# Optimization experiments

Hardware: AMD Instinct MI355X
Metric: run time of the kernel (lower is better)

## Reference

```python
import jax, jax.numpy as jnp
import numpy as np

ADMP = 8  # admp_channel -> K = ADMP*ADMP keypoints


def setup_inputs() -> dict:
    key = jax.random.key(0)
    kA, kB = jax.random.split(key)
    B, C, H, W = 8, 512, 96, 96
    feature_A = jax.random.normal(kA, (B, C, H, W), dtype=jnp.float32)
    feature_B = jax.random.normal(kB, (B, C, H, W), dtype=jnp.float32)
    return {"feature_A": feature_A, "feature_B": feature_B}


def _keypoint_rowcol(feature_A):
    # featureSelect: sum over channels, AdaptiveMaxPool2d(ADMP) with return_indices.
    # H,W divisible by ADMP so adaptive pool == uniform non-overlapping pooling.
    B, C, H, W = feature_A.shape
    ph, pw = H // ADMP, W // ADMP
    resp = feature_A.sum(axis=1)  # [B,H,W]
    r = resp.reshape(B, ADMP, ph, ADMP, pw).transpose(0, 1, 3, 2, 4)
    r = r.reshape(B, ADMP * ADMP, ph * pw)
    loc = jnp.argmax(r, axis=-1)  # first-max, matches torch  [B,K]
    kk = jnp.arange(ADMP * ADMP)
    gi, gj = kk // ADMP, kk % ADMP
    row_A = gi[None, :] * ph + loc // pw  # [B,K]
    col_A = gj[None, :] * pw + loc % pw
    return row_A, col_A


def reference(feature_A, feature_B):
    B, C, H, W = feature_A.shape
    K = ADMP * ADMP
    row_A, col_A = _keypoint_rowcol(feature_A)
    flat_A = row_A * W + col_A  # [B,K]

    # gather descriptors: [B,K,C]
    fa = feature_A.reshape(B, C, H * W)
    desc = jnp.take_along_axis(fa, flat_A[:, None, :], axis=2).transpose(0, 2, 1)

    # squared L2 distance map via ||b||^2 - 2 a.b + ||a||^2 : [B,K,HW]
    fb = feature_B.reshape(B, C, H * W)
    fb_sq = jnp.sum(fb * fb, axis=1)            # [B,HW]
    d_sq = jnp.sum(desc * desc, axis=-1)        # [B,K]
    cross = jnp.einsum('bkc,bcn->bkn', desc, fb)  # [B,K,HW]
    dist = fb_sq[:, None, :] - 2.0 * cross + d_sq[:, :, None]

    min_idx = jnp.argmin(dist, axis=-1)  # [B,K]
    row_B = min_idx // W
    col_B = min_idx % W
    drow = -(row_B - row_A)
    dcol = -(col_B - col_A)
    off = jnp.stack([drow, dcol], axis=-1)  # [B,K,2] int

    # getTranslationalOffsetByMode: most frequent (drow,dcol) pair per batch
    eq = jnp.all(off[:, :, None, :] == off[:, None, :, :], axis=-1)  # [B,K,K]
    counts = eq.sum(axis=-1)  # [B,K]
    best = jnp.argmax(counts, axis=-1)  # first occurrence on ties, matches dict order
    out = jnp.take_along_axis(off, best[:, None, None], axis=1)[:, 0, :]  # [B,2]
    return out
```

## Files before the change

kernel.cpp:

```cpp
#include <hip/hip_runtime.h>
#include <hip/hip_bf16.h>
#include <math.h>

typedef _Float16 half8 __attribute__((ext_vector_type(8)));
typedef __fp16 fp16x2 __attribute__((ext_vector_type(2)));
typedef float f32x4 __attribute__((ext_vector_type(4)));
typedef unsigned short u16x4 __attribute__((ext_vector_type(4)));
typedef unsigned short u16x8 __attribute__((ext_vector_type(8)));
typedef unsigned long long u64;

#define B_   8
#define C_   512
#define H_   96
#define W_   96
#define HW   9216
#define K_   64
#define PH   12
#define PW   12
#define NT   96
#define CCH  32
#define NBLK 96

#define OFF_PARTIAL 0u
#define OFF_DESCH   2359296u
#define OFF_DESCL   2883584u
#define OFF_ROWA    3407872u
#define OFF_COLA    3409920u
#define OFF_SLOTS   3411968u

#define FBT_LO 3072
#define BUFHW  6144

__global__ __launch_bounds__(256) void k_partial(const float* __restrict__ A,
                                                 float* __restrict__ part,
                                                 u64* __restrict__ slots) {
    if (blockIdx.x == 0 && blockIdx.y == 0) {
        slots[threadIdx.x] = ~0ull;
        slots[threadIdx.x + 256] = ~0ull;
    }
    int bxs = (blockIdx.x & 7) * 9 + (blockIdx.x >> 3);
    int idx4 = bxs * 256 + threadIdx.x;
    int chunk = blockIdx.y;
    int b = idx4 / (HW / 4), hw4 = idx4 - b * (HW / 4);
    const float* p = A + ((size_t)(b * C_ + chunk * 64)) * HW + hw4 * 4;
    float4 s = make_float4(0.f, 0.f, 0.f, 0.f);
#pragma unroll
    for (int i = 0; i < 64; ++i) {
        float4 v = *(const float4*)&p[(size_t)i * HW];
        s.x += v.x; s.y += v.y; s.z += v.z; s.w += v.w;
    }
    *(float4*)&part[chunk * (B_ * HW) + b * HW + hw4 * 4] = s;
}

__global__ void k_selgather(const float* __restrict__ part, const float* __restrict__ A,
                            int* __restrict__ rowA, int* __restrict__ colA,
                            _Float16* __restrict__ descH, _Float16* __restrict__ descL) {
    int k = blockIdx.x, b = blockIdx.y, lane = threadIdx.x;
    int gi = k >> 3, gj = k & 7;
    float bv = -1e30f; int bp = 1 << 20;
    for (int p = lane; p < PH * PW; p += 64) {
        int lr = p / PW, lc = p - lr * PW;
        int hw = (gi * PH + lr) * W_ + gj * PW + lc;
        float v = 0.f;
#pragma unroll
        for (int ch = 0; ch < 8; ++ch) v += part[ch * (B_ * HW) + b * HW + hw];
        if (v > bv || (v == bv && p < bp)) { bv = v; bp = p; }
    }
    for (int m = 1; m < 64; m <<= 1) {
        float ov = __shfl_xor(bv, m);
        int   op = __shfl_xor(bp, m);
        if (ov > bv || (ov == bv && op < bp)) { bv = ov; bp = op; }
    }
    int lr = bp / PW, lc = bp - lr * PW;
    int r = gi * PH + lr, c = gj * PW + lc;
    int flat = r * W_ + c;
    if (lane == 0) { rowA[b * K_ + k] = r; colA[b * K_ + k] = c; }
#pragma unroll
    for (int i = 0; i < 8; ++i) {
        int cc = i * 64 + lane;
        float v = A[((size_t)(b * C_ + cc)) * HW + flat];
        _Float16 h = (_Float16)v;
        _Float16 lo = (_Float16)((v - (float)h) * 2048.f);
        size_t o = ((size_t)(b * K_ + k)) * C_ + cc;
        descH[o] = h; descL[o] = lo;
    }
}

__global__ __launch_bounds__(256, 3) void k_main(const float* __restrict__ FB,
                                                 const _Float16* __restrict__ descH,
                                                 const _Float16* __restrict__ descL,
                                                 u64* __restrict__ slots) {
    __shared__ __attribute__((aligned(16))) unsigned short smem_us[2 * BUFHW];
    int b = blockIdx.y;
    int bxs = (blockIdx.x & 7) * 12 + (blockIdx.x >> 3);
    int nb = bxs * NT;
    int tid = threadIdx.x;
    int l = tid & 63;
    int w = tid >> 6;
    const size_t baseB = (size_t)b * C_ * HW + nb;

    const int so = tid % 12;
    const int scb = tid / 12;
    const int st_nt = so >> 1, st_nn0 = (so & 1) * 8;
    const size_t dbase = ((size_t)(b * K_) + w * 16 + (l & 15)) * C_ + (l >> 4) * 8;

    f32x4 accH[6], accX[6];
#pragma unroll
    for (int nt = 0; nt < 6; ++nt) {
        accH[nt] = (f32x4){0.f, 0.f, 0.f, 0.f};
        accX[nt] = (f32x4){0.f, 0.f, 0.f, 0.f};
    }
    float sq[8];
#pragma unroll
    for (int j = 0; j < 8; ++j) sq[j] = 0.f;

    float4 r0a, r0b, r1a, r1b;
    u16x8 AdH, AdL, BdH, BdL;

#define LOADFB(c0)                                                            \
    do {                                                                      \
        if (tid < 192) {                                                      \
            const float* p0 = &FB[baseB + (size_t)((c0) + scb) * HW + so * 8];      \
            const float* p1 = &FB[baseB + (size_t)((c0) + scb + 16) * HW + so * 8]; \
            r0a = *(const float4*)p0; r0b = *(const float4*)(p0 + 4);         \
            r1a = *(const float4*)p1; r1b = *(const float4*)(p1 + 4);         \
        }                                                                     \
    } while (0)

#define LOADDESC(S, c0)                                                       \
    do {                                                                      \
        S##dH = *(const u16x8*)&descH[dbase + (c0)];                          \
        S##dL = *(const u16x8*)&descL[dbase + (c0)];                          \
    } while (0)

#define CVT8(va, vb, hofs)                                                    \
    do {                                                                      \
        union { fp16x2 p[4]; half8 h; } hh, ll;                               \
        float vv[8] = {va.x, va.y, va.z, va.w, vb.x, vb.y, vb.z, vb.w};       \
        _Pragma("unroll")                                                     \
        for (int j = 0; j < 4; ++j) {                                         \
            float a = vv[2 * j], bq = vv[2 * j + 1];                          \
            fp16x2 hp = __builtin_amdgcn_cvt_pkrtz(a, bq);                    \
            float ha = (float)hp[0], hb = (float)hp[1];                       \
            fp16x2 lp = __builtin_amdgcn_cvt_pkrtz((a - ha) * 2048.f,         \
                                                   (bq - hb) * 2048.f);       \
            hh.p[j] = hp; ll.p[j] = lp;                                       \
            sq[2 * j]     = fmaf(a, a, sq[2 * j]);                            \
            sq[2 * j + 1] = fmaf(bq, bq, sq[2 * j + 1]);                      \
        }                                                                     \
        *(half8*)&smem_us[(hofs)] = hh.h;                                     \
        *(half8*)&smem_us[(hofs) + FBT_LO] = ll.h;                            \
    } while (0)

#define WRITEFB(bufhw)                                                        \
    do {                                                                      \
        if (tid < 192) {                                                      \
            int c = scb;                                                      \
            int off0 = (bufhw) + st_nt * 512 + ((c >> 2) & 1) * 256           \
                       + (c >> 3) * 64 + (c & 3) * 16 + st_nn0;               \
            CVT8(r0a, r0b, off0);                                             \
            c = scb + 16;                                                     \
            int off1 = (bufhw) + st_nt * 512 + ((c >> 2) & 1) * 256           \
                       + (c >> 3) * 64 + (c & 3) * 16 + st_nn0;               \
            CVT8(r1a, r1b, off1);                                             \
        }                                                                     \
    } while (0)

    const unsigned lds0 = (unsigned)(size_t)&smem_us[0];

#define TRQ(d0, d1, d2, d3, addr)                                             \
    asm volatile("ds_read_b64_tr_b16 %0, %1"             : "=v"(d0) : "v"(addr)); \
    asm volatile("ds_read_b64_tr_b16 %0, %1 offset:512"  : "=v"(d1) : "v"(addr)); \
    asm volatile("ds_read_b64_tr_b16 %0, %1 offset:6144" : "=v"(d2) : "v"(addr)); \
    asm volatile("ds_read_b64_tr_b16 %0, %1 offset:6656" : "=v"(d3) : "v"(addr));

#define WAIT8 asm volatile("s_waitcnt lgkmcnt(8)" ::: "memory");              \
              __builtin_amdgcn_sched_barrier(0);
#define WAIT4 asm volatile("s_waitcnt lgkmcnt(4)" ::: "memory");              \
              __builtin_amdgcn_sched_barrier(0);
#define WAIT0 asm volatile("s_waitcnt lgkmcnt(0)" ::: "memory");              \
              __builtin_amdgcn_sched_barrier(0);

#define MFMA3(nt, h0_, h1_, l0_, l1_)                                         \
    do {                                                                      \
        union { u16x4 q[2]; half8 h; } bh, bl;                                \
        bh.q[0] = h0_; bh.q[1] = h1_; bl.q[0] = l0_; bl.q[1] = l1_;           \
        accH[nt] = __builtin_amdgcn_mfma_f32_16x16x32_f16(aHu.h, bh.h, accH[nt], 0, 0, 0); \
        accX[nt] = __builtin_amdgcn_mfma_f32_16x16x32_f16(aHu.h, bl.h, accX[nt], 0, 0, 0); \
        accX[nt] = __builtin_amdgcn_mfma_f32_16x16x32_f16(aLu.h, bh.h, accX[nt], 0, 0, 0); \
    } while (0)

#define COMPUTE(cur, S)                                                       \
    do {                                                                      \
        union { u16x8 u; half8 h; } aHu, aLu;                                 \
        aHu.u = S##dH; aLu.u = S##dL;                                         \
        __builtin_amdgcn_s_setprio(1);                                        \
        const unsigned trb = lds0 + (unsigned)(cur) * 2u + (unsigned)l * 8u;  \
        u16x4 xh0, xh1, xl0, xl1, yh0, yh1, yl0, yl1, zh0, zh1, zl0, zl1;     \
        TRQ(xh0, xh1, xl0, xl1, trb);                                         \
        TRQ(yh0, yh1, yl0, yl1, trb + 1024u);                                 \
        TRQ(zh0, zh1, zl0, zl1, trb + 2048u);                                 \
        WAIT8;                                                                \
        MFMA3(0, xh0, xh1, xl0, xl1);                                         \
        TRQ(xh0, xh1, xl0, xl1, trb + 3072u);                                 \
        WAIT8;                                                                \
        MFMA3(1, yh0, yh1, yl0, yl1);                                         \
        TRQ(yh0, yh1, yl0, yl1, trb + 4096u);                                 \
        WAIT8;                                                                \
        MFMA3(2, zh0, zh1, zl0, zl1);                                         \
        TRQ(zh0, zh1, zl0, zl1, trb + 5120u);                                 \
        WAIT8;                                                                \
        MFMA3(3, xh0, xh1, xl0, xl1);                                         \
        WAIT4;                                                                \
        MFMA3(4, yh0, yh1, yl0, yl1);                                         \
        WAIT0;                                                                \
        MFMA3(5, zh0, zh1, zl0, zl1);                                         \
        __builtin_amdgcn_s_setprio(0);                                        \
    } while (0)

    LOADFB(0);
    LOADDESC(A, 0);
    LOADDESC(B, CCH);
    WRITEFB(0);
    __syncthreads();

#pragma unroll 1
    for (int tp = 0; tp < 8; ++tp) {
        const int t0 = 2 * tp, t1 = 2 * tp + 1;
        LOADFB((t0 + 1) * CCH);
        COMPUTE(0, A);
        if (t0 + 2 < 16) LOADDESC(A, (t0 + 2) * CCH);
        WRITEFB(BUFHW);
        __syncthreads();
        if (t1 + 1 < 16) LOADFB((t1 + 1) * CCH);
        COMPUTE(BUFHW, B);
        if (t1 + 2 < 16) LOADDESC(B, (t1 + 2) * CCH);
        if (t1 + 1 < 16) WRITEFB(0);
        __syncthreads();
    }

    float* fscr = (float*)&smem_us[0];
    if (tid < 192) {
        *(float4*)&fscr[scb * 96 + so * 8]     = make_float4(sq[0], sq[1], sq[2], sq[3]);
        *(float4*)&fscr[scb * 96 + so * 8 + 4] = make_float4(sq[4], sq[5], sq[6], sq[7]);
    }
    __syncthreads();
    if (tid < 96) {
        float s = 0.f;
#pragma unroll
        for (int g = 0; g < 16; ++g) s += fscr[g * 96 + tid];
        fscr[1536 + tid] = s;
    }
    __syncthreads();

    const float inv2048 = 1.f / 2048.f;
#pragma unroll
    for (int r = 0; r < 4; ++r) {
        float bv = 1e30f; int bn = 1 << 28;
#pragma unroll
        for (int nt = 0; nt < 6; ++nt) {
            float cross = accH[nt][r] + accX[nt][r] * inv2048;
            float d = fscr[1536 + nt * 16 + (l & 15)] - 2.f * cross;
            int n = nb + nt * 16 + (l & 15);
            if (d < bv) { bv = d; bn = n; }
        }
#pragma unroll
        for (int m = 1; m < 16; m <<= 1) {
            float ov = __shfl_xor(bv, m);
            int   on = __shfl_xor(bn, m);
            if (ov < bv || (ov == bv && on < bn)) { bv = ov; bn = on; }
        }
        if ((l & 15) == 0) {
            int k = w * 16 + (l >> 4) * 4 + r;
            unsigned bits = __float_as_uint(bv);
            unsigned key = (bits & 0x80000000u) ? ~bits : (bits | 0x80000000u);
            u64 packed = ((u64)key << 32) | (unsigned)bn;
            atomicMin(&slots[b * K_ + k], packed);
        }
    }
#undef LOADFB
#undef LOADDESC
#undef CVT8
#undef WRITEFB
#undef TRQ
#undef WAIT8
#undef WAIT4
#undef WAIT0
#undef MFMA3
#undef COMPUTE
}

__global__ void k_redmode(const u64* __restrict__ slots,
                          const int* __restrict__ rowA, const int* __restrict__ colA,
                          int* __restrict__ out) {
    __shared__ int r_s[64], c_s[64];
    int b = blockIdx.x, k = threadIdx.x;
    u64 s = slots[b * K_ + k];
    int bn = (int)(unsigned)(s & 0xFFFFFFFFull);
    int rB = bn / W_, cB = bn - rB * W_;
    r_s[k] = rowA[b * K_ + k] - rB;
    c_s[k] = colA[b * K_ + k] - cB;
    __syncthreads();
    int mr = r_s[k], mc = c_s[k], cnt = 0;
#pragma unroll
    for (int j = 0; j < 64; ++j) cnt += (r_s[j] == mr && c_s[j] == mc) ? 1 : 0;
    int bk = k, bc = cnt;
    for (int m = 1; m < 64; m <<= 1) {
        int oc = __shfl_xor(bc, m);
        int ok = __shfl_xor(bk, m);
        if (oc > bc || (oc == bc && ok < bk)) { bc = oc; bk = ok; }
    }
    if (k == 0) { out[b * 2] = r_s[bk]; out[b * 2 + 1] = c_s[bk]; }
}

extern "C" void kernel_launch(void* const* d_in, const int* in_sizes, int n_in,
                              void* d_out, int out_size, void* d_ws, size_t ws_size,
                              hipStream_t stream) {
    const float* A  = (const float*)d_in[0];
    const float* FB = (const float*)d_in[1];
    char* ws = (char*)d_ws;
    float*     part  = (float*)(ws + OFF_PARTIAL);
    _Float16*  descH = (_Float16*)(ws + OFF_DESCH);
    _Float16*  descL = (_Float16*)(ws + OFF_DESCL);
    int*       rowA  = (int*)(ws + OFF_ROWA);
    int*       colA  = (int*)(ws + OFF_COLA);
    u64*       slots = (u64*)(ws + OFF_SLOTS);
    int*       out   = (int*)d_out;

    k_partial<<<dim3((B_ * HW) / 1024, 8), 256, 0, stream>>>(A, part, slots);
    k_selgather<<<dim3(K_, B_), 64, 0, stream>>>(part, A, rowA, colA, descH, descL);
    k_main<<<dim3(NBLK, B_), 256, 0, stream>>>(FB, descH, descL, slots);
    k_redmode<<<dim3(B_), 64, 0, stream>>>(slots, rowA, colA, out);
}
```

Before: 81.99 us.

## Retile main distance kernel to 64-pixel blocks with all-K per wave

```diff
diff --git a/kernel.cpp b/kernel.cpp
--- a/kernel.cpp
+++ b/kernel.cpp
@@ -17,9 +17,9 @@
 #define K_   64
 #define PH   12
 #define PW   12
-#define NT   96
+#define NT   64
 #define CCH  32
-#define NBLK 96
+#define NBLK 144
 
 #define OFF_PARTIAL 0u
 #define OFF_DESCH   2359296u
@@ -28,8 +28,8 @@
 #define OFF_COLA    3409920u
 #define OFF_SLOTS   3411968u
 
-#define FBT_LO 3072
-#define BUFHW  6144
+#define FBT_LO 2048
+#define BUFHW  4096
 
 __global__ __launch_bounds__(256) void k_partial(const float* __restrict__ A,
                                                  float* __restrict__ part,
@@ -92,51 +92,55 @@
                                                  u64* __restrict__ slots) {
     __shared__ __attribute__((aligned(16))) unsigned short smem_us[2 * BUFHW];
     int b = blockIdx.y;
-    int bxs = (blockIdx.x & 7) * 12 + (blockIdx.x >> 3);
+    int bxs = (blockIdx.x & 7) * 18 + (blockIdx.x >> 3);
     int nb = bxs * NT;
     int tid = threadIdx.x;
     int l = tid & 63;
     int w = tid >> 6;
     const size_t baseB = (size_t)b * C_ * HW + nb;
 
-    const int so = tid % 12;
-    const int scb = tid / 12;
-    const int st_nt = so >> 1, st_nn0 = (so & 1) * 8;
-    const size_t dbase = ((size_t)(b * K_) + w * 16 + (l & 15)) * C_ + (l >> 4) * 8;
-
-    f32x4 accH[6], accX[6];
-#pragma unroll
-    for (int nt = 0; nt < 6; ++nt) {
-        accH[nt] = (f32x4){0.f, 0.f, 0.f, 0.f};
-        accX[nt] = (f32x4){0.f, 0.f, 0.f, 0.f};
+    const int o_ = tid & 7;
+    const int cr = tid >> 3;
+    const int stb = (o_ >> 1) * 512 + ((cr >> 2) & 1) * 256 + (cr >> 3) * 64
+                    + (cr & 3) * 16 + (o_ & 1) * 8;
+    const size_t dbase = ((size_t)(b * K_) + (l & 15)) * C_ + (l >> 4) * 8;
+
+    f32x4 accH[4], accX[4];
+#pragma unroll
+    for (int mt = 0; mt < 4; ++mt) {
+        accH[mt] = (f32x4){0.f, 0.f, 0.f, 0.f};
+        accX[mt] = (f32x4){0.f, 0.f, 0.f, 0.f};
     }
     float sq[8];
 #pragma unroll
     for (int j = 0; j < 8; ++j) sq[j] = 0.f;
 
-    float4 r0a, r0b, r1a, r1b;
-    u16x8 AdH, AdL, BdH, BdL;
+    float4 f0_, f1_;
+    u16x8 AdH0, AdH1, AdH2, AdH3, AdL0, AdL1, AdL2, AdL3;
+    u16x8 BdH0, BdH1, BdH2, BdH3, BdL0, BdL1, BdL2, BdL3;
 
 #define LOADFB(c0)                                                            \
     do {                                                                      \
-        if (tid < 192) {                                                      \
-            const float* p0 = &FB[baseB + (size_t)((c0) + scb) * HW + so * 8];      \
-            const float* p1 = &FB[baseB + (size_t)((c0) + scb + 16) * HW + so * 8]; \
-            r0a = *(const float4*)p0; r0b = *(const float4*)(p0 + 4);         \
-            r1a = *(const float4*)p1; r1b = *(const float4*)(p1 + 4);         \
-        }                                                                     \
+        const float* p0 = &FB[baseB + (size_t)((c0) + cr) * HW + o_ * 8];     \
+        f0_ = *(const float4*)p0; f1_ = *(const float4*)(p0 + 4);             \
     } while (0)
 
 #define LOADDESC(S, c0)                                                       \
     do {                                                                      \
-        S##dH = *(const u16x8*)&descH[dbase + (c0)];                          \
-        S##dL = *(const u16x8*)&descL[dbase + (c0)];                          \
-    } while (0)
-
-#define CVT8(va, vb, hofs)                                                    \
+        S##dH0 = *(const u16x8*)&descH[dbase + (c0)];                         \
+        S##dL0 = *(const u16x8*)&descL[dbase + (c0)];                         \
+        S##dH1 = *(const u16x8*)&descH[dbase + 16 * C_ + (c0)];               \
+        S##dL1 = *(const u16x8*)&descL[dbase + 16 * C_ + (c0)];               \
+        S##dH2 = *(const u16x8*)&descH[dbase + 32 * C_ + (c0)];               \
+        S##dL2 = *(const u16x8*)&descL[dbase + 32 * C_ + (c0)];               \
+        S##dH3 = *(const u16x8*)&descH[dbase + 48 * C_ + (c0)];               \
+        S##dL3 = *(const u16x8*)&descL[dbase + 48 * C_ + (c0)];               \
+    } while (0)
+
+#define WRITEFB(bufhw)                                                        \
     do {                                                                      \
         union { fp16x2 p[4]; half8 h; } hh, ll;                               \
-        float vv[8] = {va.x, va.y, va.z, va.w, vb.x, vb.y, vb.z, vb.w};       \
+        float vv[8] = {f0_.x, f0_.y, f0_.z, f0_.w, f1_.x, f1_.y, f1_.z, f1_.w}; \
         _Pragma("unroll")                                                     \
         for (int j = 0; j < 4; ++j) {                                         \
             float a = vv[2 * j], bq = vv[2 * j + 1];                          \
@@ -148,80 +152,48 @@
             sq[2 * j]     = fmaf(a, a, sq[2 * j]);                            \
             sq[2 * j + 1] = fmaf(bq, bq, sq[2 * j + 1]);                      \
         }                                                                     \
-        *(half8*)&smem_us[(hofs)] = hh.h;                                     \
-        *(half8*)&smem_us[(hofs) + FBT_LO] = ll.h;                            \
-    } while (0)
-
-#define WRITEFB(bufhw)                                                        \
-    do {                                                                      \
-        if (tid < 192) {                                                      \
-            int c = scb;                                                      \
-            int off0 = (bufhw) + st_nt * 512 + ((c >> 2) & 1) * 256           \
-                       + (c >> 3) * 64 + (c & 3) * 16 + st_nn0;               \
-            CVT8(r0a, r0b, off0);                                             \
-            c = scb + 16;                                                     \
-            int off1 = (bufhw) + st_nt * 512 + ((c >> 2) & 1) * 256           \
-                       + (c >> 3) * 64 + (c & 3) * 16 + st_nn0;               \
-            CVT8(r1a, r1b, off1);                                             \
-        }                                                                     \
+        *(half8*)&smem_us[(bufhw) + stb] = hh.h;                              \
+        *(half8*)&smem_us[(bufhw) + stb + FBT_LO] = ll.h;                     \
     } while (0)
 
     const unsigned lds0 = (unsigned)(size_t)&smem_us[0];
 
-#define TRQ(d0, d1, d2, d3, addr)                                             \
-    asm volatile("ds_read_b64_tr_b16 %0, %1"             : "=v"(d0) : "v"(addr)); \
-    asm volatile("ds_read_b64_tr_b16 %0, %1 offset:512"  : "=v"(d1) : "v"(addr)); \
-    asm volatile("ds_read_b64_tr_b16 %0, %1 offset:6144" : "=v"(d2) : "v"(addr)); \
-    asm volatile("ds_read_b64_tr_b16 %0, %1 offset:6656" : "=v"(d3) : "v"(addr));
-
-#define WAIT8 asm volatile("s_waitcnt lgkmcnt(8)" ::: "memory");              \
-              __builtin_amdgcn_sched_barrier(0);
-#define WAIT4 asm volatile("s_waitcnt lgkmcnt(4)" ::: "memory");              \
-              __builtin_amdgcn_sched_barrier(0);
 #define WAIT0 asm volatile("s_waitcnt lgkmcnt(0)" ::: "memory");              \
               __builtin_amdgcn_sched_barrier(0);
 
-#define MFMA3(nt, h0_, h1_, l0_, l1_)                                         \
-    do {                                                                      \
+#define MFMA3(mt, AH, AL)                                                     \
+    do {                                                                      \
+        union { u16x8 u; half8 h; } ah, al;                                   \
+        ah.u = AH; al.u = AL;                                                 \
+        accH[mt] = __builtin_amdgcn_mfma_f32_16x16x32_f16(ah.h, bh.h, accH[mt], 0, 0, 0); \
+        accX[mt] = __builtin_amdgcn_mfma_f32_16x16x32_f16(ah.h, bl.h, accX[mt], 0, 0, 0); \
+        accX[mt] = __builtin_amdgcn_mfma_f32_16x16x32_f16(al.h, bh.h, accX[mt], 0, 0, 0); \
+    } while (0)
+
+#define COMPUTE(cur, S)                                                       \
+    do {                                                                      \
+        const unsigned trb = lds0 + (unsigned)(cur) * 2u                      \
+                             + (unsigned)w * 1024u + (unsigned)l * 8u;        \
+        u16x4 h0, h1, q0, q1;                                                 \
+        asm volatile("ds_read_b64_tr_b16 %0, %1"             : "=v"(h0) : "v"(trb)); \
+        asm volatile("ds_read_b64_tr_b16 %0, %1 offset:512"  : "=v"(h1) : "v"(trb)); \
+        asm volatile("ds_read_b64_tr_b16 %0, %1 offset:4096" : "=v"(q0) : "v"(trb)); \
+        asm volatile("ds_read_b64_tr_b16 %0, %1 offset:4608" : "=v"(q1) : "v"(trb)); \
+        WAIT0;                                                                \
         union { u16x4 q[2]; half8 h; } bh, bl;                                \
-        bh.q[0] = h0_; bh.q[1] = h1_; bl.q[0] = l0_; bl.q[1] = l1_;           \
-        accH[nt] = __builtin_amdgcn_mfma_f32_16x16x32_f16(aHu.h, bh.h, accH[nt], 0, 0, 0); \
-        accX[nt] = __builtin_amdgcn_mfma_f32_16x16x32_f16(aHu.h, bl.h, accX[nt], 0, 0, 0); \
-        accX[nt] = __builtin_amdgcn_mfma_f32_16x16x32_f16(aLu.h, bh.h, accX[nt], 0, 0, 0); \
-    } while (0)
-
-#define COMPUTE(cur, S)                                                       \
-    do {                                                                      \
-        union { u16x8 u; half8 h; } aHu, aLu;                                 \
-        aHu.u = S##dH; aLu.u = S##dL;                                         \
+        bh.q[0] = h0; bh.q[1] = h1; bl.q[0] = q0; bl.q[1] = q1;               \
         __builtin_amdgcn_s_setprio(1);                                        \
-        const unsigned trb = lds0 + (unsigned)(cur) * 2u + (unsigned)l * 8u;  \
-        u16x4 xh0, xh1, xl0, xl1, yh0, yh1, yl0, yl1, zh0, zh1, zl0, zl1;     \
-        TRQ(xh0, xh1, xl0, xl1, trb);                                         \
-        TRQ(yh0, yh1, yl0, yl1, trb + 1024u);                                 \
-        TRQ(zh0, zh1, zl0, zl1, trb + 2048u);                                 \
-        WAIT8;                                                                \
-        MFMA3(0, xh0, xh1, xl0, xl1);                                         \
-        TRQ(xh0, xh1, xl0, xl1, trb + 3072u);                                 \
-        WAIT8;                                                                \
-        MFMA3(1, yh0, yh1, yl0, yl1);                                         \
-        TRQ(yh0, yh1, yl0, yl1, trb + 4096u);                                 \
-        WAIT8;                                                                \
-        MFMA3(2, zh0, zh1, zl0, zl1);                                         \
-        TRQ(zh0, zh1, zl0, zl1, trb + 5120u);                                 \
-        WAIT8;                                                                \
-        MFMA3(3, xh0, xh1, xl0, xl1);                                         \
-        WAIT4;                                                                \
-        MFMA3(4, yh0, yh1, yl0, yl1);                                         \
-        WAIT0;                                                                \
-        MFMA3(5, zh0, zh1, zl0, zl1);                                         \
+        MFMA3(0, S##dH0, S##dL0);                                             \
+        MFMA3(1, S##dH1, S##dL1);                                             \
+        MFMA3(2, S##dH2, S##dL2);                                             \
+        MFMA3(3, S##dH3, S##dL3);                                             \
         __builtin_amdgcn_s_setprio(0);                                        \
     } while (0)
 
     LOADFB(0);
     LOADDESC(A, 0);
+    WRITEFB(0);
     LOADDESC(B, CCH);
-    WRITEFB(0);
     __syncthreads();
 
 #pragma unroll 1
@@ -240,51 +212,59 @@
     }
 
     float* fscr = (float*)&smem_us[0];
-    if (tid < 192) {
-        *(float4*)&fscr[scb * 96 + so * 8]     = make_float4(sq[0], sq[1], sq[2], sq[3]);
-        *(float4*)&fscr[scb * 96 + so * 8 + 4] = make_float4(sq[4], sq[5], sq[6], sq[7]);
-    }
-    __syncthreads();
-    if (tid < 96) {
+    float* fsq_s = (float*)&smem_us[2 * BUFHW - 0] - 2048;
+    float* bvs = fsq_s + 64;
+    int*   bns = (int*)(fsq_s + 64 + 256);
+    *(float4*)&fscr[cr * 64 + o_ * 8]     = make_float4(sq[0], sq[1], sq[2], sq[3]);
+    *(float4*)&fscr[cr * 64 + o_ * 8 + 4] = make_float4(sq[4], sq[5], sq[6], sq[7]);
+    __syncthreads();
+    if (tid < 64) {
         float s = 0.f;
 #pragma unroll
-        for (int g = 0; g < 16; ++g) s += fscr[g * 96 + tid];
-        fscr[1536 + tid] = s;
+        for (int g = 0; g < 32; ++g) s += fscr[g * 64 + tid];
+        fsq_s[tid] = s;
     }
     __syncthreads();
 
     const float inv2048 = 1.f / 2048.f;
-#pragma unroll
-    for (int r = 0; r < 4; ++r) {
+    const float fsq = fsq_s[w * 16 + (l & 15)];
+#pragma unroll
+    for (int mt = 0; mt < 4; ++mt) {
+#pragma unroll
+        for (int r = 0; r < 4; ++r) {
+            float cross = accH[mt][r] + accX[mt][r] * inv2048;
+            float bv = fsq - 2.f * cross;
+            int bn = nb + w * 16 + (l & 15);
+#pragma unroll
+            for (int m = 1; m < 16; m <<= 1) {
+                float ov = __shfl_xor(bv, m);
+                int   on = __shfl_xor(bn, m);
+                if (ov < bv || (ov == bv && on < bn)) { bv = ov; bn = on; }
+            }
+            if ((l & 15) == 0) {
+                int k = mt * 16 + (l >> 4) * 4 + r;
+                bvs[k * 4 + w] = bv;
+                bns[k * 4 + w] = bn;
+            }
+        }
+    }
+    __syncthreads();
+    if (tid < K_) {
         float bv = 1e30f; int bn = 1 << 28;
 #pragma unroll
-        for (int nt = 0; nt < 6; ++nt) {
-            float cross = accH[nt][r] + accX[nt][r] * inv2048;
-            float d = fscr[1536 + nt * 16 + (l & 15)] - 2.f * cross;
-            int n = nb + nt * 16 + (l & 15);
-            if (d < bv) { bv = d; bn = n; }
-        }
-#pragma unroll
-        for (int m = 1; m < 16; m <<= 1) {
-            float ov = __shfl_xor(bv, m);
-            int   on = __shfl_xor(bn, m);
+        for (int j = 0; j < 4; ++j) {
+            float ov = bvs[tid * 4 + j];
+            int   on = bns[tid * 4 + j];
             if (ov < bv || (ov == bv && on < bn)) { bv = ov; bn = on; }
         }
-        if ((l & 15) == 0) {
-            int k = w * 16 + (l >> 4) * 4 + r;
-            unsigned bits = __float_as_uint(bv);
-            unsigned key = (bits & 0x80000000u) ? ~bits : (bits | 0x80000000u);
-            u64 packed = ((u64)key << 32) | (unsigned)bn;
-            atomicMin(&slots[b * K_ + k], packed);
-        }
+        unsigned bits = __float_as_uint(bv);
+        unsigned key = (bits & 0x80000000u) ? ~bits : (bits | 0x80000000u);
+        u64 packed = ((u64)key << 32) | (unsigned)bn;
+        atomicMin(&slots[b * K_ + tid], packed);
     }
 #undef LOADFB
 #undef LOADDESC
-#undef CVT8
 #undef WRITEFB
-#undef TRQ
-#undef WAIT8
-#undef WAIT4
 #undef WAIT0
 #undef MFMA3
 #undef COMPUTE
```

New measurement: 132.0 us. +61.0%, slower.
